# Kernel tuning notes

Hardware: AMD Instinct MI355X
Metric: run time of the kernel (lower is better)

The kernel has to match this reference:

```python
import jax, jax.numpy as jnp
import numpy as np


def sinusoidal_pe(S, D, dtype):
    # standard transformer sinusoidal positional encoding, shape [S, D]
    pos = jnp.arange(S, dtype=jnp.float32)[:, None]
    div = jnp.exp(jnp.arange(0, D, 2, dtype=jnp.float32) * (-np.log(10000.0) / D))
    ang = pos * div  # [S, D/2]
    pe = jnp.zeros((S, D), jnp.float32)
    pe = pe.at[:, 0::2].set(jnp.sin(ang)).at[:, 1::2].set(jnp.cos(ang))
    return pe.astype(dtype)


def setup_inputs() -> dict:
    key = jax.random.key(0)
    k1, k2, k3, k4, k5 = jax.random.split(key, 5)
    B, S, F, D, SEG = 64, 512, 64, 1024, 8
    x = jax.random.normal(k1, (B, S, F), jnp.float32)
    W_emb = jax.random.normal(k2, (F, D), jnp.float32) / np.sqrt(F)
    b_emb = jax.random.normal(k3, (D,), jnp.float32) * 0.01
    w_seg = jax.random.normal(k4, (SEG,), jnp.float32) / np.sqrt(SEG)
    b_seg = jax.random.normal(k5, (1,), jnp.float32) * 0.01
    return {"x": x, "W_emb": W_emb, "b_emb": b_emb, "w_seg": w_seg, "b_seg": b_seg}


def reference(x, W_emb, b_emb, w_seg, b_seg):
    B, S, F = x.shape
    D = W_emb.shape[1]
    seg_len = w_seg.shape[0]  # seq_len divisible by seg_len -> pad_len == 0 branch
    # input token embedding
    x1 = x @ W_emb + b_emb  # [B, S, D]
    # segment embedding: tensor_split at multiples of seg_len == reshape,
    # Linear(seg_len, 1) over the time axis of each chunk, broadcast over chunk.
    xr = x1.reshape(B, S // seg_len, seg_len, D)
    seg = jnp.einsum('bnsd,s->bnd', xr, w_seg) + b_seg[0]  # [B, n_seg, D]
    x2 = (xr + seg[:, :, None, :]).reshape(B, S, D)
    # positional encoding added to x2
    return x2 + sinusoidal_pe(S, D, x2.dtype)
```

## Files before the change

kernel.cpp:

```cpp
#include <hip/hip_runtime.h>
#include <stdint.h>


typedef __attribute__((ext_vector_type(8))) short short8;
typedef __attribute__((ext_vector_type(4))) float f32x4;

#define D_DIM 1024
#define BM 64
#define BN 128

__device__ __forceinline__ unsigned short f2bf(float f) {
  unsigned u = __float_as_uint(f);
  u = (u + 0x7FFFu + ((u >> 16) & 1u)) >> 16;
  return (unsigned short)u;
}

__global__ __launch_bounds__(256) void bert_input_kernel(
    const float* __restrict__ x, const float* __restrict__ W,
    const float* __restrict__ b_emb, const float* __restrict__ w_seg,
    const float* __restrict__ b_seg, float* __restrict__ out) {
  __shared__ unsigned short ldsb[8 * 2 * 64 * 8];

  const int tid = threadIdx.x;
  const int lane = tid & 63;
  const int wave = tid >> 6;
  const int bid = blockIdx.x;
  const int nblk = bid & 7;
  const int mblk = bid >> 3;
  const int nbase = nblk * BN;
  const int mbase = mblk * BM;

  {
    const int k = tid >> 2;
    const int cq = (tid & 3) * 4;
    const int kf = k >> 5;
    const int j = k & 7;
    const int laneb = ((k >> 3) & 3) << 4;
    const float4* wrow =
        reinterpret_cast<const float4*>(W + (size_t)k * D_DIM + nbase);
#pragma unroll
    for (int q = 0; q < 8; ++q) {
      int c = cq + q * 16;
      float4 v = wrow[c >> 2];
      int nf = c >> 4;
      int base = ((nf * 2 + kf) * 64 + (laneb | (c & 15))) * 8 + j;
      ldsb[base + 0 * 8] = f2bf(v.x);
      ldsb[base + 1 * 8] = f2bf(v.y);
      ldsb[base + 2 * 8] = f2bf(v.z);
      ldsb[base + 3 * 8] = f2bf(v.w);
    }
  }

  float Sw = 0.f;
#pragma unroll
  for (int i = 0; i < 8; ++i) Sw += w_seg[i];
  const int g = lane >> 4;
  float wl[4];
#pragma unroll
  for (int j = 0; j < 4; ++j) wl[j] = w_seg[(g & 1) * 4 + j];
  const float bseg = b_seg[0];

  const int mw = wave >> 1;
  const int nw = wave & 1;
  short8 afrag[2][2];
  {
    const int row0 = mbase + mw * 32 + (lane & 15);
    const int k0 = (lane >> 4) * 8;
#pragma unroll
    for (int mf = 0; mf < 2; ++mf) {
#pragma unroll
      for (int kf = 0; kf < 2; ++kf) {
        const float* p = x + (size_t)(row0 + mf * 16) * 64 + kf * 32 + k0;
        float4 v0 = *reinterpret_cast<const float4*>(p);
        float4 v1 = *reinterpret_cast<const float4*>(p + 4);
        short8 a;
        a[0] = (short)f2bf(v0.x); a[1] = (short)f2bf(v0.y);
        a[2] = (short)f2bf(v0.z); a[3] = (short)f2bf(v0.w);
        a[4] = (short)f2bf(v1.x); a[5] = (short)f2bf(v1.y);
        a[6] = (short)f2bf(v1.z); a[7] = (short)f2bf(v1.w);
        afrag[mf][kf] = a;
      }
    }
  }

  __syncthreads();

  short8 bfrag[4][2];
#pragma unroll
  for (int nf = 0; nf < 4; ++nf) {
#pragma unroll
    for (int kf = 0; kf < 2; ++kf) {
      int nfg = nw * 4 + nf;
      bfrag[nf][kf] = *reinterpret_cast<const short8*>(
          &ldsb[((nfg * 2 + kf) * 64 + lane) * 8]);
    }
  }

  f32x4 acc[2][4];
#pragma unroll
  for (int mf = 0; mf < 2; ++mf) {
#pragma unroll
    for (int nf = 0; nf < 4; ++nf) {
      f32x4 c = {0.f, 0.f, 0.f, 0.f};
      c = __builtin_amdgcn_mfma_f32_16x16x32_bf16(afrag[mf][0], bfrag[nf][0],
                                                  c, 0, 0, 0);
      c = __builtin_amdgcn_mfma_f32_16x16x32_bf16(afrag[mf][1], bfrag[nf][1],
                                                  c, 0, 0, 0);
      acc[mf][nf] = c;
    }
  }

  const float inv2pi = 0.15915494309189535f;
  const float KLOG = 0.02595256324130752f;

#pragma unroll
  for (int nf = 0; nf < 4; ++nf) {
    const int col = nbase + (nw * 4 + nf) * 16 + (lane & 15);
    const float cconst = b_emb[col] * (1.f + Sw) + bseg;
    const float divrev = exp2f(-(float)(col >> 1) * KLOG) * inv2pi;
    const float qshift = (col & 1) ? 0.25f : 0.f;
#pragma unroll
    for (int mf = 0; mf < 2; ++mf) {
      f32x4 a = acc[mf][nf];
      float p = wl[0] * a[0] + wl[1] * a[1] + wl[2] * a[2] + wl[3] * a[3];
      p += __shfl_xor(p, 16);
      const int rbase = mbase + mw * 32 + mf * 16 + g * 4;
      const int sbase = rbase & 511;
#pragma unroll
      for (int j = 0; j < 4; ++j) {
        float rev = (float)(sbase + j) * divrev + qshift;
        rev = rev - floorf(rev);
        float pe = __builtin_amdgcn_sinf(rev);
        out[(size_t)(rbase + j) * D_DIM + col] = a[j] + p + cconst + pe;
      }
    }
  }
}

extern "C" void kernel_launch(void* const* d_in, const int* in_sizes, int n_in,
                              void* d_out, int out_size, void* d_ws,
                              size_t ws_size, hipStream_t stream) {
  const float* x = (const float*)d_in[0];
  const float* W = (const float*)d_in[1];
  const float* b_emb = (const float*)d_in[2];
  const float* w_seg = (const float*)d_in[3];
  const float* b_seg = (const float*)d_in[4];
  float* out = (float*)d_out;

  dim3 grid(4096);
  dim3 block(256);
  bert_input_kernel<<<grid, block, 0, stream>>>(x, W, b_emb, w_seg, b_seg,
                                                out);
}
```

Before: 37.95 us.

## Split into setup prepack kernel and transposed-MFMA main kernel with float4 stores

Adds a setup kernel that converts x and W to bf16 in MFMA fragment order and precomputes a per-(position, column) table holding the sinusoidal encoding plus the folded bias terms. The main kernel swaps MFMA operands so each lane owns four consecutive columns, which allows 16-byte output stores. The segment reduction moves to xor-shuffles across rows, and the main kernel reads the precomputed table instead of evaluating sin. It also remaps block indices and drops the LDS staging. The cost is a second launch plus about 2MB of extra table traffic, in exchange for fewer redundant conversions and wider stores.

```diff
diff --git a/kernel.cpp b/kernel.cpp
--- a/kernel.cpp
+++ b/kernel.cpp
@@ -6,8 +6,8 @@
 typedef __attribute__((ext_vector_type(4))) float f32x4;
 
 #define D_DIM 1024
-#define BM 64
-#define BN 128
+#define WS_PE_OFF 131072
+#define WS_X_OFF (131072 + 2097152)
 
 __device__ __forceinline__ unsigned short f2bf(float f) {
   unsigned u = __float_as_uint(f);
@@ -15,124 +15,131 @@
   return (unsigned short)u;
 }
 
-__global__ __launch_bounds__(256) void bert_input_kernel(
+__global__ __launch_bounds__(256) void bert_setup_kernel(
     const float* __restrict__ x, const float* __restrict__ W,
     const float* __restrict__ b_emb, const float* __restrict__ w_seg,
-    const float* __restrict__ b_seg, float* __restrict__ out) {
-  __shared__ unsigned short ldsb[8 * 2 * 64 * 8];
+    const float* __restrict__ b_seg, unsigned short* __restrict__ wsW,
+    float* __restrict__ wsPE, unsigned short* __restrict__ wsX) {
+  const int bid = blockIdx.x;
+  const int tid = threadIdx.x;
+  if (bid < 1024) {
+    const int t = bid * 256 + tid;
+    const float4* p = reinterpret_cast<const float4*>(x) + (size_t)t * 2;
+    float4 v0 = p[0], v1 = p[1];
+    short8 o;
+    o[0] = (short)f2bf(v0.x); o[1] = (short)f2bf(v0.y);
+    o[2] = (short)f2bf(v0.z); o[3] = (short)f2bf(v0.w);
+    o[4] = (short)f2bf(v1.x); o[5] = (short)f2bf(v1.y);
+    o[6] = (short)f2bf(v1.z); o[7] = (short)f2bf(v1.w);
+    *reinterpret_cast<short8*>(wsX + (size_t)t * 8) = o;
+  } else if (bid < 3072) {
+    const int t = (bid - 1024) * 256 + tid;
+    const int s = t >> 10;
+    const int c = t & 1023;
+    float Sw = 0.f;
+#pragma unroll
+    for (int i = 0; i < 8; ++i) Sw += w_seg[i];
+    const float inv2pi = 0.15915494309189535f;
+    const float KLOG = 0.02595256324130752f;
+    float divrev = exp2f(-(float)(c >> 1) * KLOG) * inv2pi;
+    float rev = (float)s * divrev + ((c & 1) ? 0.25f : 0.f);
+    rev = rev - floorf(rev);
+    float pe = __builtin_amdgcn_sinf(rev);
+    wsPE[t] = pe + b_emb[c] * (1.f + Sw) + b_seg[0];
+  } else {
+    const int t = (bid - 3072) * 256 + tid;
+    const int cf = t >> 7;
+    const int kf = (t >> 6) & 1;
+    const int lane = t & 63;
+    const int col = cf * 16 + (lane & 15);
+    const int k0 = kf * 32 + ((lane >> 4) << 3);
+    short8 o;
+#pragma unroll
+    for (int i = 0; i < 8; ++i)
+      o[i] = (short)f2bf(W[(size_t)(k0 + i) * D_DIM + col]);
+    *reinterpret_cast<short8*>(wsW + (size_t)t * 8) = o;
+  }
+}
 
+__global__ __launch_bounds__(256) void bert_main_kernel(
+    const unsigned short* __restrict__ wsX,
+    const unsigned short* __restrict__ wsW, const float* __restrict__ wsPE,
+    const float* __restrict__ w_seg, float* __restrict__ out) {
   const int tid = threadIdx.x;
   const int lane = tid & 63;
   const int wave = tid >> 6;
   const int bid = blockIdx.x;
-  const int nblk = bid & 7;
-  const int mblk = bid >> 3;
-  const int nbase = nblk * BN;
-  const int mbase = mblk * BM;
+  const int nblk = (bid >> 3) & 7;
+  const int mblk = (bid & 7) | ((bid >> 6) << 3);
+  const int mbase = mblk * 64;
+  const int nbase = nblk * 128;
+  const int mw = wave >> 1;
+  const int nw = wave & 1;
+  const int L15 = lane & 15;
+  const int g = lane >> 4;
 
-  {
-    const int k = tid >> 2;
-    const int cq = (tid & 3) * 4;
-    const int kf = k >> 5;
-    const int j = k & 7;
-    const int laneb = ((k >> 3) & 3) << 4;
-    const float4* wrow =
-        reinterpret_cast<const float4*>(W + (size_t)k * D_DIM + nbase);
+  short8 aW[4][2];
 #pragma unroll
-    for (int q = 0; q < 8; ++q) {
-      int c = cq + q * 16;
-      float4 v = wrow[c >> 2];
-      int nf = c >> 4;
-      int base = ((nf * 2 + kf) * 64 + (laneb | (c & 15))) * 8 + j;
-      ldsb[base + 0 * 8] = f2bf(v.x);
-      ldsb[base + 1 * 8] = f2bf(v.y);
-      ldsb[base + 2 * 8] = f2bf(v.z);
-      ldsb[base + 3 * 8] = f2bf(v.w);
+  for (int cf = 0; cf < 4; ++cf) {
+#pragma unroll
+    for (int kf = 0; kf < 2; ++kf) {
+      const int cfg = (nbase >> 4) + nw * 4 + cf;
+      aW[cf][kf] = *reinterpret_cast<const short8*>(
+          wsW + ((size_t)(cfg * 2 + kf) * 64 + lane) * 8);
     }
   }
 
-  float Sw = 0.f;
+  short8 bX[2][2];
 #pragma unroll
-  for (int i = 0; i < 8; ++i) Sw += w_seg[i];
-  const int g = lane >> 4;
-  float wl[4];
+  for (int rf = 0; rf < 2; ++rf) {
 #pragma unroll
-  for (int j = 0; j < 4; ++j) wl[j] = w_seg[(g & 1) * 4 + j];
-  const float bseg = b_seg[0];
-
-  const int mw = wave >> 1;
-  const int nw = wave & 1;
-  short8 afrag[2][2];
-  {
-    const int row0 = mbase + mw * 32 + (lane & 15);
-    const int k0 = (lane >> 4) * 8;
-#pragma unroll
-    for (int mf = 0; mf < 2; ++mf) {
-#pragma unroll
-      for (int kf = 0; kf < 2; ++kf) {
-        const float* p = x + (size_t)(row0 + mf * 16) * 64 + kf * 32 + k0;
-        float4 v0 = *reinterpret_cast<const float4*>(p);
-        float4 v1 = *reinterpret_cast<const float4*>(p + 4);
-        short8 a;
-        a[0] = (short)f2bf(v0.x); a[1] = (short)f2bf(v0.y);
-        a[2] = (short)f2bf(v0.z); a[3] = (short)f2bf(v0.w);
-        a[4] = (short)f2bf(v1.x); a[5] = (short)f2bf(v1.y);
-        a[6] = (short)f2bf(v1.z); a[7] = (short)f2bf(v1.w);
-        afrag[mf][kf] = a;
-      }
+    for (int kf = 0; kf < 2; ++kf) {
+      const int row = mbase + mw * 32 + rf * 16 + L15;
+      bX[rf][kf] = *reinterpret_cast<const short8*>(
+          wsX + (size_t)row * 64 + kf * 32 + g * 8);
     }
   }
 
-  __syncthreads();
-
-  short8 bfrag[4][2];
+  f32x4 acc[4][2];
 #pragma unroll
-  for (int nf = 0; nf < 4; ++nf) {
+  for (int cf = 0; cf < 4; ++cf) {
 #pragma unroll
-    for (int kf = 0; kf < 2; ++kf) {
-      int nfg = nw * 4 + nf;
-      bfrag[nf][kf] = *reinterpret_cast<const short8*>(
-          &ldsb[((nfg * 2 + kf) * 64 + lane) * 8]);
+    for (int rf = 0; rf < 2; ++rf) {
+      f32x4 c = {0.f, 0.f, 0.f, 0.f};
+      c = __builtin_amdgcn_mfma_f32_16x16x32_bf16(aW[cf][0], bX[rf][0], c, 0,
+                                                  0, 0);
+      c = __builtin_amdgcn_mfma_f32_16x16x32_bf16(aW[cf][1], bX[rf][1], c, 0,
+                                                  0, 0);
+      acc[cf][rf] = c;
     }
   }
 
-  f32x4 acc[2][4];
-#pragma unroll
-  for (int mf = 0; mf < 2; ++mf) {
-#pragma unroll
-    for (int nf = 0; nf < 4; ++nf) {
-      f32x4 c = {0.f, 0.f, 0.f, 0.f};
-      c = __builtin_amdgcn_mfma_f32_16x16x32_bf16(afrag[mf][0], bfrag[nf][0],
-                                                  c, 0, 0, 0);
-      c = __builtin_amdgcn_mfma_f32_16x16x32_bf16(afrag[mf][1], bfrag[nf][1],
-                                                  c, 0, 0, 0);
-      acc[mf][nf] = c;
-    }
-  }
-
-  const float inv2pi = 0.15915494309189535f;
-  const float KLOG = 0.02595256324130752f;
+  const float t = w_seg[lane & 7];
 
 #pragma unroll
-  for (int nf = 0; nf < 4; ++nf) {
-    const int col = nbase + (nw * 4 + nf) * 16 + (lane & 15);
-    const float cconst = b_emb[col] * (1.f + Sw) + bseg;
-    const float divrev = exp2f(-(float)(col >> 1) * KLOG) * inv2pi;
-    const float qshift = (col & 1) ? 0.25f : 0.f;
+  for (int cf = 0; cf < 4; ++cf) {
 #pragma unroll
-    for (int mf = 0; mf < 2; ++mf) {
-      f32x4 a = acc[mf][nf];
-      float p = wl[0] * a[0] + wl[1] * a[1] + wl[2] * a[2] + wl[3] * a[3];
-      p += __shfl_xor(p, 16);
-      const int rbase = mbase + mw * 32 + mf * 16 + g * 4;
-      const int sbase = rbase & 511;
-#pragma unroll
-      for (int j = 0; j < 4; ++j) {
-        float rev = (float)(sbase + j) * divrev + qshift;
-        rev = rev - floorf(rev);
-        float pe = __builtin_amdgcn_sinf(rev);
-        out[(size_t)(rbase + j) * D_DIM + col] = a[j] + p + cconst + pe;
-      }
+    for (int rf = 0; rf < 2; ++rf) {
+      f32x4 a = acc[cf][rf];
+      float q0 = a[0] * t, q1 = a[1] * t, q2 = a[2] * t, q3 = a[3] * t;
+      q0 += __shfl_xor(q0, 1); q1 += __shfl_xor(q1, 1);
+      q2 += __shfl_xor(q2, 1); q3 += __shfl_xor(q3, 1);
+      q0 += __shfl_xor(q0, 2); q1 += __shfl_xor(q1, 2);
+      q2 += __shfl_xor(q2, 2); q3 += __shfl_xor(q3, 2);
+      q0 += __shfl_xor(q0, 4); q1 += __shfl_xor(q1, 4);
+      q2 += __shfl_xor(q2, 4); q3 += __shfl_xor(q3, 4);
+
+      const int row = mbase + mw * 32 + rf * 16 + L15;
+      const int s = row & 511;
+      const int colq = nbase + nw * 64 + cf * 16 + g * 4;
+      const float4 pe4 =
+          *reinterpret_cast<const float4*>(wsPE + (size_t)s * D_DIM + colq);
+      float4 o;
+      o.x = a[0] + q0 + pe4.x;
+      o.y = a[1] + q1 + pe4.y;
+      o.z = a[2] + q2 + pe4.z;
+      o.w = a[3] + q3 + pe4.w;
+      *reinterpret_cast<float4*>(out + (size_t)row * D_DIM + colq) = o;
     }
   }
 }
@@ -147,8 +154,11 @@
   const float* b_seg = (const float*)d_in[4];
   float* out = (float*)d_out;
 
-  dim3 grid(4096);
-  dim3 block(256);
-  bert_input_kernel<<<grid, block, 0, stream>>>(x, W, b_emb, w_seg, b_seg,
-                                                out);
+  unsigned short* wsW = (unsigned short*)d_ws;
+  float* wsPE = (float*)((char*)d_ws + WS_PE_OFF);
+  unsigned short* wsX = (unsigned short*)((char*)d_ws + WS_X_OFF);
+
+  bert_setup_kernel<<<3104, 256, 0, stream>>>(x, W, b_emb, w_seg, b_seg, wsW,
+                                              wsPE, wsX);
+  bert_main_kernel<<<4096, 256, 0, stream>>>(wsX, wsW, wsPE, w_seg, out);
 }
```

Measured after the change: 46.86 us. 1.23x slower.
